# Kernel optimization log

Measured on AMD Instinct MI355X. Metric: run time of the kernel, lower is better.

Reference implementation:

```python
import jax, jax.numpy as jnp
import numpy as np

B, T, D, H, L, E, K = 4, 1024, 1024, 16, 2, 8, 2
HD = D // H                      # head_dim = 64
HALF = HD // 2                   # rope half dim = 32
CAP = int(np.ceil(2.0 * B * T / E))  # capacity factor 2 -> 1024
EPS = 1e-5


def build_sin_cos(seq_len, half_dim):
    pos = jnp.arange(seq_len, dtype=jnp.float32)[:, None]
    inv_freq = 1.0 / (10000.0 ** (jnp.arange(0, half_dim * 2, 2, dtype=jnp.float32) / (half_dim * 2)))
    ang = pos * inv_freq                      # (T, half_dim)
    return jnp.sin(ang), jnp.cos(ang)


def layernorm(x, g, b):
    mu = jnp.mean(x, -1, keepdims=True)
    var = jnp.mean(jnp.square(x - mu), -1, keepdims=True)
    return (x - mu) * jax.lax.rsqrt(var + EPS) * g + b


def attention(x, qkv_w, proj_w, sin, cos):
    # x: (B,T,D)
    qkv = (x @ qkv_w).reshape(B, T, H, 3 * HD)
    q, k, v = jnp.split(qkv, 3, axis=-1)      # each (B,T,H,HD)
    s = sin[None, :, None, :]                 # (1,T,1,HALF)
    c = cos[None, :, None, :]
    def rope(t):
        t1, t2 = t[..., :HALF], t[..., HALF:]
        return jnp.concatenate([t1 * c - t2 * s, t1 * s + t2 * c], axis=-1)
    q, k = rope(q), rope(k)
    scores = jnp.einsum('bqhd,bkhd->bhqk', q, k) / jnp.sqrt(jnp.float32(HD)).astype(x.dtype)
    causal = jnp.tril(jnp.ones((T, T), dtype=bool))
    scores = jnp.where(causal, scores, jnp.asarray(-1e9, scores.dtype))
    probs = jax.nn.softmax(scores, axis=-1)
    out = jnp.einsum('bhqk,bkhd->bqhd', probs, v).reshape(B, T, D)
    return out @ proj_w


def sparse_moe(x, gate_w, w1, b1, w2, b2):
    # eval mode: no router noise, aux_loss = 0
    flat = x.reshape(-1, D)                   # (N, D)
    N = flat.shape[0]
    gates = jax.nn.softmax((flat @ gate_w).astype(jnp.float32), axis=-1)  # (N, E)
    _, inds = jax.lax.top_k(gates, K)         # (N, K)
    mask = jnp.zeros((N, E), dtype=bool).at[jnp.arange(N)[:, None], inds].set(True)
    pos = jnp.cumsum(mask.astype(jnp.int32), axis=0) * mask - 1
    keep = (pos < CAP) & mask                 # (N, E) capacity-truncated assignment
    keepT = keep.T                            # (E, N)
    # stable argsort puts kept tokens first, preserving token order
    order = jnp.argsort(~keepT, axis=1)[:, :CAP]           # (E, CAP)
    valid = jnp.take_along_axis(keepT, order, axis=1)      # (E, CAP)
    safe = jnp.where(valid, order, 0)
    xg = flat[safe]                                        # (E, CAP, D)
    gv = jnp.take_along_axis(gates.T, safe, axis=1) * valid  # (E, CAP)
    h = jax.nn.gelu(jnp.einsum('ecd,edh->ech', xg, w1) + b1[:, None, :], approximate=False)
    out = jnp.einsum('ech,ehd->ecd', h, w2) + b2[:, None, :]
    contrib = out * gv[..., None].astype(flat.dtype)
    scatter_idx = jnp.where(valid, order, N)               # out-of-range -> dropped
    final = jnp.zeros_like(flat).at[scatter_idx.reshape(-1)].add(
        contrib.reshape(-1, D), mode='drop')
    return final.reshape(x.shape)


def setup_inputs() -> dict:
    key = jax.random.key(0)
    ks = jax.random.split(key, 8)
    s = 0.02
    return {
        'x': jax.random.normal(ks[0], (B, T, D), jnp.float32),
        'ln1_g': jnp.ones((L, D), jnp.float32),
        'ln1_b': jnp.zeros((L, D), jnp.float32),
        'qkv_w': jax.random.normal(ks[1], (L, D, 3 * D), jnp.float32) * s,
        'proj_w': jax.random.normal(ks[2], (L, D, D), jnp.float32) * s,
        'ln2_g': jnp.ones((L, D), jnp.float32),
        'ln2_b': jnp.zeros((L, D), jnp.float32),
        'gate_w': jax.random.normal(ks[3], (L, D, E), jnp.float32) * s,
        'w1': jax.random.normal(ks[4], (L, E, D, 4 * D), jnp.float32) * s,
        'b1': jnp.zeros((L, E, 4 * D), jnp.float32),
        'w2': jax.random.normal(ks[5], (L, E, 4 * D, D), jnp.float32) * s,
        'b2': jnp.zeros((L, E, D), jnp.float32),
    }


def reference(x, ln1_g, ln1_b, qkv_w, proj_w, ln2_g, ln2_b, gate_w, w1, b1, w2, b2):
    sin, cos = build_sin_cos(T, HALF)
    for l in range(L):
        x = x + attention(layernorm(x, ln1_g[l], ln1_b[l]), qkv_w[l], proj_w[l], sin, cos)
        x = x + sparse_moe(layernorm(x, ln2_g[l], ln2_b[l]), gate_w[l], w1[l], b1[l], w2[l], b2[l])
    return x
```

## Files before the change

### kernel.cpp

```cpp
#include <hip/hip_runtime.h>
#include <cstdint>

#define DD 1024
#define TT 1024
#define BB 4
#define HH 16
#define EE 8
#define NTOK 4096
#define CAPS 1024

using f16 = _Float16;
using f16x8 = __attribute__((ext_vector_type(8))) _Float16;
using f16x4 = __attribute__((ext_vector_type(4))) _Float16;
using f32x4 = __attribute__((ext_vector_type(4))) float;

#define MFMA16(a, b, c) __builtin_amdgcn_mfma_f32_16x16x32_f16(a, b, c, 0, 0, 0)

__device__ __forceinline__ void gload16(const void* g, void* l) {
  __builtin_amdgcn_global_load_lds((const __attribute__((address_space(1))) unsigned int*)g,
                                   (__attribute__((address_space(3))) unsigned int*)l, 16, 0, 0);
}

__device__ __forceinline__ void split2(float v, f16& h, f16& lo) {
  h = (f16)v;
  lo = (f16)((v - (float)h) * 2048.0f);
}

__device__ __forceinline__ void split_store(f16* ph, f16* pl, float v) {
  f16 h = (f16)v;
  *ph = h;
  *pl = (f16)((v - (float)h) * 2048.0f);
}

__global__ void splitT_k(const float* __restrict__ src, f16* __restrict__ dh, f16* __restrict__ dl,
                         int R, int C, long sSrc, long sDst) {
  __shared__ float tile[32][33];
  long z = blockIdx.z;
  src += z * sSrc; dh += z * sDst; dl += z * sDst;
  int c0 = blockIdx.x * 32, r0 = blockIdx.y * 32;
  int tx = threadIdx.x, ty = threadIdx.y;
  #pragma unroll
  for (int i = 0; i < 4; ++i) {
    int r = ty + i * 8;
    tile[r][tx] = src[(long)(r0 + r) * C + c0 + tx];
  }
  __syncthreads();
  #pragma unroll
  for (int i = 0; i < 4; ++i) {
    int cc = ty + i * 8;
    float v = tile[tx][cc];
    long idx = (long)(c0 + cc) * R + r0 + tx;
    f16 h, lo; split2(v, h, lo);
    dh[idx] = h; dl[idx] = lo;
  }
}

template<bool GATE>
__launch_bounds__(256)
__global__ void ln_k(const float* __restrict__ x, const float* __restrict__ g, const float* __restrict__ b,
                     f16* __restrict__ oh, f16* __restrict__ ol,
                     const float* __restrict__ gw, float* __restrict__ gates) {
  int row = blockIdx.x, tid = threadIdx.x;
  int lane = tid & 63, wid = tid >> 6;
  __shared__ float red[4];
  __shared__ float pg[4][8];
  __shared__ float logits[8];
  const float* xr = x + (long)row * DD;
  int col = tid * 4;
  float4 v = *(const float4*)(xr + col);
  float s = v.x + v.y + v.z + v.w;
  #pragma unroll
  for (int off = 32; off >= 1; off >>= 1) s += __shfl_down(s, off);
  if (lane == 0) red[wid] = s;
  __syncthreads();
  float mu = (red[0] + red[1] + red[2] + red[3]) * (1.0f / DD);
  float d0 = v.x - mu, d1 = v.y - mu, d2 = v.z - mu, d3 = v.w - mu;
  float sq = d0 * d0 + d1 * d1 + d2 * d2 + d3 * d3;
  __syncthreads();
  #pragma unroll
  for (int off = 32; off >= 1; off >>= 1) sq += __shfl_down(sq, off);
  if (lane == 0) red[wid] = sq;
  __syncthreads();
  float var = (red[0] + red[1] + red[2] + red[3]) * (1.0f / DD);
  float rstd = rsqrtf(var + 1e-5f);
  float xv[4];
  xv[0] = d0 * rstd * g[col] + b[col];
  xv[1] = d1 * rstd * g[col + 1] + b[col + 1];
  xv[2] = d2 * rstd * g[col + 2] + b[col + 2];
  xv[3] = d3 * rstd * g[col + 3] + b[col + 3];
  f16x4 hv, lv;
  #pragma unroll
  for (int j = 0; j < 4; ++j) { f16 h, lo; split2(xv[j], h, lo); hv[j] = h; lv[j] = lo; }
  *(f16x4*)(oh + (long)row * DD + col) = hv;
  *(f16x4*)(ol + (long)row * DD + col) = lv;
  if (GATE) {
    float part[8];
    #pragma unroll
    for (int e = 0; e < 8; ++e) part[e] = 0.0f;
    #pragma unroll
    for (int j = 0; j < 4; ++j) {
      const float* gwr = gw + (long)(col + j) * 8;
      #pragma unroll
      for (int e = 0; e < 8; ++e) part[e] += xv[j] * gwr[e];
    }
    #pragma unroll
    for (int off = 32; off >= 1; off >>= 1) {
      #pragma unroll
      for (int e = 0; e < 8; ++e) part[e] += __shfl_down(part[e], off);
    }
    if (lane == 0) {
      #pragma unroll
      for (int e = 0; e < 8; ++e) pg[wid][e] = part[e];
    }
    __syncthreads();
    if (tid < 8) logits[tid] = pg[0][tid] + pg[1][tid] + pg[2][tid] + pg[3][tid];
    __syncthreads();
    if (tid < 8) {
      float mx = logits[0];
      #pragma unroll
      for (int e2 = 1; e2 < 8; ++e2) mx = fmaxf(mx, logits[e2]);
      float den = 0.0f;
      #pragma unroll
      for (int e2 = 0; e2 < 8; ++e2) den += expf(logits[e2] - mx);
      gates[(long)row * 8 + tid] = expf(logits[tid] - mx) / den;
    }
  }
}

__global__ void sincos_k(float* st, float* ct) {
  int i = blockIdx.x * 256 + threadIdx.x;
  if (i >= TT * 32) return;
  int t = i >> 5, f = i & 31;
  float inv = powf(10000.0f, -(float)f * (1.0f / 32.0f));
  float ang = (float)t * inv;
  st[i] = sinf(ang);
  ct[i] = cosf(ang);
}

__launch_bounds__(256)
__global__ void rope_split_k(const float* __restrict__ qkv, const float* __restrict__ st, const float* __restrict__ ct,
                             f16* __restrict__ qh, f16* __restrict__ ql,
                             f16* __restrict__ kh, f16* __restrict__ kl,
                             f16* __restrict__ vth, f16* __restrict__ vtl) {
  int bx = blockIdx.x;
  int bh = bx >> 4, t0 = (bx & 15) * 64;
  int b = bh >> 4, hh = bh & 15;
  int tid = threadIdx.x;
  {
    int r = tid >> 2, quarter = tid & 3;
    int t = t0 + r;
    const float* rowp = qkv + ((long)(b * TT + t)) * 3072 + hh * 192;
    long obase = ((long)bh * TT + t) * 64;
    #pragma unroll
    for (int j = 0; j < 8; ++j) {
      int i = quarter * 8 + j;
      float sa = st[t * 32 + i], ca = ct[t * 32 + i];
      float a1 = rowp[i], a2 = rowp[i + 32];
      split_store(qh + obase + i, ql + obase + i, a1 * ca - a2 * sa);
      split_store(qh + obase + i + 32, ql + obase + i + 32, a1 * sa + a2 * ca);
      float c1 = rowp[64 + i], c2 = rowp[96 + i];
      split_store(kh + obase + i, kl + obase + i, c1 * ca - c2 * sa);
      split_store(kh + obase + i + 32, kl + obase + i + 32, c1 * sa + c2 * ca);
    }
  }
  __shared__ f16 vh_t[64][72];
  __shared__ f16 vl_t[64][72];
  {
    int d = tid & 63, tq = tid >> 6;
    #pragma unroll
    for (int p = 0; p < 16; ++p) {
      int tl = tq * 16 + p;
      float val = qkv[((long)(b * TT + t0 + tl)) * 3072 + hh * 192 + 128 + d];
      f16 h, lo; split2(val, h, lo);
      vh_t[tl][d] = h; vl_t[tl][d] = lo;
    }
  }
  __syncthreads();
  {
    int d = tid >> 2, c = tid & 3;
    long vbase = ((long)bh * 64 + d) * TT + t0 + c * 16;
    f16x8 ph0, ph1, pl0, pl1;
    #pragma unroll
    for (int j = 0; j < 8; ++j) {
      ph0[j] = vh_t[c * 16 + j][d];
      pl0[j] = vl_t[c * 16 + j][d];
      ph1[j] = vh_t[c * 16 + 8 + j][d];
      pl1[j] = vl_t[c * 16 + 8 + j][d];
    }
    *(f16x8*)(vth + vbase) = ph0;
    *(f16x8*)(vth + vbase + 8) = ph1;
    *(f16x8*)(vtl + vbase) = pl0;
    *(f16x8*)(vtl + vbase + 8) = pl1;
  }
}

__launch_bounds__(256)
__global__ void attn_k(const f16* __restrict__ qh, const f16* __restrict__ ql,
                       const f16* __restrict__ kh, const f16* __restrict__ kl,
                       const f16* __restrict__ vth, const f16* __restrict__ vtl,
                       f16* __restrict__ oh_out, f16* __restrict__ ol_out) {
  int bx = blockIdx.x;
  int bh = bx >> 4, qt = bx & 15;
  int tid = threadIdx.x;
  int wid = tid >> 6, lane = tid & 63;
  int lr = lane & 15, lg = lane >> 4;
  int qbase = qt * 64 + wid * 16;
  long bhT = (long)bh * TT;

  long qoff = (bhT + qbase + lr) * 64 + lg * 8;
  f16x8 q_h0 = *(const f16x8*)(qh + qoff);
  f16x8 q_h1 = *(const f16x8*)(qh + qoff + 32);
  f16x8 q_l0 = *(const f16x8*)(ql + qoff);
  f16x8 q_l1 = *(const f16x8*)(ql + qoff + 32);

  f32x4 o_hi[4], o_md[4];
  #pragma unroll
  for (int d = 0; d < 4; ++d) {
    o_hi[d] = {0.f, 0.f, 0.f, 0.f};
    o_md[d] = {0.f, 0.f, 0.f, 0.f};
  }
  float m[4], lsum[4];
  #pragma unroll
  for (int j = 0; j < 4; ++j) { m[j] = -1e30f; lsum[j] = 0.0f; }

  __shared__ f16 Ph[4][16][32];
  __shared__ f16 Pl[4][16][32];

  int ntiles = (qbase + 47) >> 5;
  for (int kb = 0; kb < ntiles; ++kb) {
    int kv0 = kb * 32;
    float sv[2][4];
    #pragma unroll
    for (int ni = 0; ni < 2; ++ni) {
      long koff = (bhT + kv0 + ni * 16 + lr) * 64 + lg * 8;
      f16x8 k_h0 = *(const f16x8*)(kh + koff);
      f16x8 k_h1 = *(const f16x8*)(kh + koff + 32);
      f16x8 k_l0 = *(const f16x8*)(kl + koff);
      f16x8 k_l1 = *(const f16x8*)(kl + koff + 32);
      f32x4 a = {0.f, 0.f, 0.f, 0.f};
      a = MFMA16(q_h0, k_h0, a);
      a = MFMA16(q_h1, k_h1, a);
      a = a * 2048.0f;
      a = MFMA16(q_h0, k_l0, a);
      a = MFMA16(q_h1, k_l1, a);
      a = MFMA16(q_l0, k_h0, a);
      a = MFMA16(q_l1, k_h1, a);
      #pragma unroll
      for (int j = 0; j < 4; ++j) sv[ni][j] = a[j];
    }
    const float sscale = 0.125f / 2048.0f;
    bool needmask = (kv0 + 32 > qbase);
    float rm[4];
    #pragma unroll
    for (int j = 0; j < 4; ++j) {
      int qrow = qbase + lg * 4 + j;
      float s0 = sv[0][j] * sscale;
      float s1 = sv[1][j] * sscale;
      if (needmask) {
        if (kv0 + lr > qrow) s0 = -1e9f;
        if (kv0 + 16 + lr > qrow) s1 = -1e9f;
      }
      sv[0][j] = s0; sv[1][j] = s1;
      rm[j] = fmaxf(s0, s1);
    }
    #pragma unroll
    for (int off = 1; off < 16; off <<= 1) {
      #pragma unroll
      for (int j = 0; j < 4; ++j) rm[j] = fmaxf(rm[j], __shfl_xor(rm[j], off));
    }
    float alpha[4], rs[4];
    #pragma unroll
    for (int j = 0; j < 4; ++j) {
      float mn = fmaxf(m[j], rm[j]);
      alpha[j] = expf(m[j] - mn);
      m[j] = mn;
      float p0 = expf(sv[0][j] - mn);
      float p1 = expf(sv[1][j] - mn);
      sv[0][j] = p0; sv[1][j] = p1;
      rs[j] = p0 + p1;
    }
    #pragma unroll
    for (int off = 1; off < 16; off <<= 1) {
      #pragma unroll
      for (int j = 0; j < 4; ++j) rs[j] += __shfl_xor(rs[j], off);
    }
    #pragma unroll
    for (int j = 0; j < 4; ++j) lsum[j] = lsum[j] * alpha[j] + rs[j];
    #pragma unroll
    for (int d = 0; d < 4; ++d) {
      #pragma unroll
      for (int j = 0; j < 4; ++j) { o_hi[d][j] *= alpha[j]; o_md[d][j] *= alpha[j]; }
    }
    #pragma unroll
    for (int ni = 0; ni < 2; ++ni) {
      #pragma unroll
      for (int j = 0; j < 4; ++j) {
        float pv = sv[ni][j];
        f16 hv = (f16)pv;
        Ph[wid][lg * 4 + j][ni * 16 + lr] = hv;
        Pl[wid][lg * 4 + j][ni * 16 + lr] = (f16)((pv - (float)hv) * 2048.0f);
      }
    }
    f16x8 pa_h = *(const f16x8*)(&Ph[wid][lr][lg * 8]);
    f16x8 pa_l = *(const f16x8*)(&Pl[wid][lr][lg * 8]);
    #pragma unroll
    for (int d = 0; d < 4; ++d) {
      long voff = ((long)bh * 64 + d * 16 + lr) * TT + kv0 + lg * 8;
      f16x8 v_h = *(const f16x8*)(vth + voff);
      f16x8 v_l = *(const f16x8*)(vtl + voff);
      o_hi[d] = MFMA16(pa_h, v_h, o_hi[d]);
      o_md[d] = MFMA16(pa_h, v_l, o_md[d]);
      o_md[d] = MFMA16(pa_l, v_h, o_md[d]);
    }
  }
  int b = bh >> 4, hh = bh & 15;
  #pragma unroll
  for (int j = 0; j < 4; ++j) {
    float invl = 1.0f / lsum[j];
    int qrow = qbase + lg * 4 + j;
    long obase = ((long)(b * TT + qrow)) * DD + hh * 64 + lr;
    #pragma unroll
    for (int d = 0; d < 4; ++d) {
      float val = (o_hi[d][j] + o_md[d][j] * (1.0f / 2048.0f)) * invl;
      f16 hv = (f16)val;
      oh_out[obase + d * 16] = hv;
      ol_out[obase + d * 16] = (f16)((val - (float)hv) * 2048.0f);
    }
  }
}

template<int EPI, bool SPLIT>
__launch_bounds__(256, 2)
__global__ void gemmF(const f16* __restrict__ Ah, const f16* __restrict__ Al, long sA,
                      const f16* __restrict__ Bh, const f16* __restrict__ Bl, long sB,
                      int M, int N, int K,
                      float* __restrict__ outF, long sOutF,
                      const float* __restrict__ resid,
                      const float* __restrict__ bias, long sBias,
                      f16* __restrict__ outH, f16* __restrict__ outL, long sOutH) {
  __shared__ __align__(16) f16 pool[(SPLIT ? 4 : 2) * 128 * 64];
  f16* AsH = pool;
  f16* BsH = pool + 8192;
  f16* AsL = SPLIT ? pool + 16384 : pool;
  f16* BsL = SPLIT ? pool + 24576 : pool;

  int z = blockIdx.z;
  int bn = blockIdx.x, bm = blockIdx.y;
  int tid = threadIdx.x;
  int wid = tid >> 6, lane = tid & 63;
  int wm = (wid >> 1) * 64, wn = (wid & 1) * 64;
  int lr = lane & 15, lg = lane >> 4;

  f32x4 aH[4][4], aL[4][4];
  #pragma unroll
  for (int i = 0; i < 4; ++i)
    #pragma unroll
    for (int j = 0; j < 4; ++j) {
      aH[i][j] = {0.f, 0.f, 0.f, 0.f};
      if (SPLIT) aL[i][j] = {0.f, 0.f, 0.f, 0.f};
    }

  int srow = tid >> 3;
  int gcol = (((tid & 7) ^ (srow & 7)) << 3);
  const f16* apH = Ah + (long)z * sA + ((long)(bm * 128 + srow)) * K + gcol;
  const f16* bpH = Bh + (long)z * sB + ((long)(bn * 128 + srow)) * K + gcol;
  const f16* apL = nullptr; const f16* bpL = nullptr;
  if (SPLIT) {
    apL = Al + (long)z * sA + ((long)(bm * 128 + srow)) * K + gcol;
    bpL = Bl + (long)z * sB + ((long)(bn * 128 + srow)) * K + gcol;
  }
  int tid8 = tid * 8;
  int rsw = lr & 7;

  for (int kt = 0; kt < K; kt += 64) {
    #pragma unroll
    for (int r4 = 0; r4 < 4; ++r4) {
      long go = (long)kt + (long)(r4 * 32) * K;
      int lo = tid8 + r4 * 2048;
      gload16(apH + go, AsH + lo);
      gload16(bpH + go, BsH + lo);
      if (SPLIT) {
        gload16(apL + go, AsL + lo);
        gload16(bpL + go, BsL + lo);
      }
    }
    __syncthreads();
    #pragma unroll
    for (int kk2 = 0; kk2 < 2; ++kk2) {
      int sws = (((kk2 << 2) | lg) ^ rsw) << 3;
      f16x8 afH[4], afL[4];
      #pragma unroll
      for (int i = 0; i < 4; ++i) {
        int ro = (wm + i * 16 + lr) * 64 + sws;
        afH[i] = *(const f16x8*)(AsH + ro);
        if (SPLIT) afL[i] = *(const f16x8*)(AsL + ro);
      }
      #pragma unroll
      for (int j = 0; j < 4; ++j) {
        int ro = (wn + j * 16 + lr) * 64 + sws;
        f16x8 bH = *(const f16x8*)(BsH + ro);
        #pragma unroll
        for (int i = 0; i < 4; ++i) aH[i][j] = MFMA16(afH[i], bH, aH[i][j]);
        if (SPLIT) {
          f16x8 bL = *(const f16x8*)(BsL + ro);
          #pragma unroll
          for (int i = 0; i < 4; ++i) {
            aL[i][j] = MFMA16(afH[i], bL, aL[i][j]);
            aL[i][j] = MFMA16(afL[i], bH, aL[i][j]);
          }
        }
      }
    }
    __syncthreads();
  }

  #pragma unroll
  for (int i = 0; i < 4; ++i) {
    #pragma unroll
    for (int j = 0; j < 4; ++j) {
      #pragma unroll
      for (int r = 0; r < 4; ++r) {
        int row = bm * 128 + wm + i * 16 + lg * 4 + r;
        int col = bn * 128 + wn + j * 16 + lr;
        float v = aH[i][j][r];
        if (SPLIT) v += aL[i][j][r] * (1.0f / 2048.0f);
        if (EPI == 0) {
          outF[(long)row * N + col] = v;
        } else if (EPI == 1) {
          long idx = (long)row * N + col;
          outF[idx] = v + resid[idx];
        } else if (EPI == 2) {
          float t = v + bias[(long)z * sBias + col];
          float ge = 0.5f * t * (1.0f + erff(t * 0.70710678118f));
          long idx = (long)z * sOutH + (long)row * N + col;
          f16 hv = (f16)ge;
          outH[idx] = hv;
          if (SPLIT) outL[idx] = (f16)((ge - (float)hv) * 2048.0f);
        } else {
          long idx = (long)z * sOutF + (long)row * N + col;
          outF[idx] = v + bias[(long)z * sBias + col];
        }
      }
    }
  }
}

__launch_bounds__(512)
__global__ void route_k(const float* __restrict__ gates, int* __restrict__ etok, int* __restrict__ slotof) {
  __shared__ unsigned char lmask[NTOK];
  __shared__ unsigned char ltop[NTOK];
  int tid = threadIdx.x;
  for (int t = tid; t < NTOK; t += 512) {
    const float* gr = gates + (long)t * 8;
    float gv[8];
    #pragma unroll
    for (int e = 0; e < 8; ++e) gv[e] = gr[e];
    int e1 = 0; float bv = gv[0];
    #pragma unroll
    for (int e = 1; e < 8; ++e) if (gv[e] > bv) { bv = gv[e]; e1 = e; }
    int e2 = -1; float bv2 = -1e30f;
    #pragma unroll
    for (int e = 0; e < 8; ++e) if (e != e1 && gv[e] > bv2) { bv2 = gv[e]; e2 = e; }
    lmask[t] = (unsigned char)((1u << e1) | (1u << e2));
    ltop[t] = (unsigned char)(e1 | (e2 << 4));
    slotof[t * 2] = -1;
    slotof[t * 2 + 1] = -1;
  }
  __syncthreads();
  int e = tid >> 6, lane = tid & 63;
  int cnt = 0;
  for (int c = 0; c < NTOK / 64; ++c) {
    int t = c * 64 + lane;
    int bit = (lmask[t] >> e) & 1;
    unsigned long long bal = __ballot(bit);
    int pre = __popcll(bal & ((1ull << lane) - 1ull));
    int slot = cnt + pre;
    if (bit && slot < CAPS) {
      etok[e * CAPS + slot] = t;
      int tp = ltop[t];
      int k = ((tp & 15) == e) ? 0 : 1;
      slotof[t * 2 + k] = (e << 16) | slot;
    }
    cnt += __popcll(bal);
  }
  int kept = cnt < CAPS ? cnt : CAPS;
  for (int s = kept + lane; s < CAPS; s += 64) etok[e * CAPS + s] = 0;
}

__global__ void gather_k(const int* __restrict__ etok, const f16* __restrict__ xh, const f16* __restrict__ xl,
                         f16* __restrict__ gh, f16* __restrict__ gl) {
  int es = blockIdx.x, tid = threadIdx.x;
  int tok = etok[es];
  const uint4* s1 = (const uint4*)(xh + (long)tok * DD);
  const uint4* s2 = (const uint4*)(xl + (long)tok * DD);
  ((uint4*)(gh + (long)es * DD))[tid] = s1[tid];
  ((uint4*)(gl + (long)es * DD))[tid] = s2[tid];
}

__global__ void scatter_k(const int* __restrict__ slotof, const float* __restrict__ gates,
                          const float* __restrict__ moe, float* __restrict__ x) {
  int t = blockIdx.x, tid = threadIdx.x;
  int s0 = slotof[t * 2], s1 = slotof[t * 2 + 1];
  float4* xr = (float4*)(x + (long)t * DD);
  float4 v = xr[tid];
  if (s0 >= 0) {
    int e = s0 >> 16, sl = s0 & 0xffff;
    float gv = gates[(long)t * 8 + e];
    float4 mo = ((const float4*)(moe + ((long)e * CAPS + sl) * DD))[tid];
    v.x += gv * mo.x; v.y += gv * mo.y; v.z += gv * mo.z; v.w += gv * mo.w;
  }
  if (s1 >= 0) {
    int e = s1 >> 16, sl = s1 & 0xffff;
    float gv = gates[(long)t * 8 + e];
    float4 mo = ((const float4*)(moe + ((long)e * CAPS + sl) * DD))[tid];
    v.x += gv * mo.x; v.y += gv * mo.y; v.z += gv * mo.z; v.w += gv * mo.w;
  }
  xr[tid] = v;
}

extern "C" void kernel_launch(void* const* d_in, const int* in_sizes, int n_in,
                              void* d_out, int out_size, void* d_ws, size_t ws_size,
                              hipStream_t stream) {
  const float* x_in   = (const float*)d_in[0];
  const float* ln1_g  = (const float*)d_in[1];
  const float* ln1_b  = (const float*)d_in[2];
  const float* qkv_w  = (const float*)d_in[3];
  const float* proj_w = (const float*)d_in[4];
  const float* ln2_g  = (const float*)d_in[5];
  const float* ln2_b  = (const float*)d_in[6];
  const float* gate_w = (const float*)d_in[7];
  const float* w1     = (const float*)d_in[8];
  const float* b1     = (const float*)d_in[9];
  const float* w2     = (const float*)d_in[10];
  const float* b2     = (const float*)d_in[11];
  float* x = (float*)d_out;

  char* p = (char*)d_ws;
  auto alloc = [&](size_t bytes) { char* r = p; p += (bytes + 255) & ~(size_t)255; return (void*)r; };

  f16* Wreg   = (f16*)alloc(134217728);
  float* qkvb = (float*)alloc(4096ull * 3072 * 4);
  f16* qhB  = (f16*)alloc(4194304ull * 2);
  f16* qlB  = (f16*)alloc(4194304ull * 2);
  f16* khB  = (f16*)alloc(4194304ull * 2);
  f16* klB  = (f16*)alloc(4194304ull * 2);
  f16* vthB = (f16*)alloc(4194304ull * 2);
  f16* vtlB = (f16*)alloc(4194304ull * 2);
  f16* xnh  = (f16*)alloc(4194304ull * 2);
  f16* xnl  = (f16*)alloc(4194304ull * 2);
  f16* atth = (f16*)alloc(4194304ull * 2);
  f16* attl = (f16*)alloc(4194304ull * 2);
  f16* xgh  = (f16*)alloc(8388608ull * 2);
  f16* xgl  = (f16*)alloc(8388608ull * 2);
  f16* hhB  = (f16*)alloc(33554432ull * 2);
  f16* hlB  = (f16*)alloc(33554432ull * 2);
  float* moe = (float*)alloc(8388608ull * 4);
  float* stab = (float*)alloc(32768ull * 4);
  float* ctab = (float*)alloc(32768ull * 4);
  float* gates = (float*)alloc(32768ull * 4);
  int* etok  = (int*)alloc(8192ull * 4);
  int* slotof = (int*)alloc(8192ull * 4);

  f16* qkvTh = Wreg;
  f16* qkvTl = Wreg + 3145728;
  f16* projTh = Wreg + 2 * 3145728;
  f16* projTl = Wreg + 2 * 3145728 + 1048576;
  f16* w1Th = Wreg;
  f16* w1Tl = Wreg + 33554432;
  f16* w2Th = Wreg;
  f16* w2Tl = Wreg + 33554432;

  hipMemcpyAsync(x, x_in, (size_t)NTOK * DD * 4, hipMemcpyDeviceToDevice, stream);
  sincos_k<<<(TT * 32 + 255) / 256, 256, 0, stream>>>(stab, ctab);

  for (int l = 0; l < 2; ++l) {
    splitT_k<<<dim3(3072 / 32, 1024 / 32, 1), dim3(32, 8), 0, stream>>>(
        qkv_w + (long)l * DD * 3072, qkvTh, qkvTl, 1024, 3072, 0, 0);
    splitT_k<<<dim3(1024 / 32, 1024 / 32, 1), dim3(32, 8), 0, stream>>>(
        proj_w + (long)l * DD * DD, projTh, projTl, 1024, 1024, 0, 0);
    ln_k<false><<<NTOK, 256, 0, stream>>>(x, ln1_g + l * DD, ln1_b + l * DD, xnh, xnl, nullptr, nullptr);
    gemmF<0, true><<<dim3(3072 / 128, 4096 / 128, 1), 256, 0, stream>>>(
        xnh, xnl, 0, qkvTh, qkvTl, 0, 4096, 3072, 1024,
        qkvb, 0, nullptr, nullptr, 0, nullptr, nullptr, 0);
    rope_split_k<<<BB * HH * (TT / 64), 256, 0, stream>>>(qkvb, stab, ctab, qhB, qlB, khB, klB, vthB, vtlB);
    attn_k<<<BB * HH * (TT / 64), 256, 0, stream>>>(qhB, qlB, khB, klB, vthB, vtlB, atth, attl);
    gemmF<1, true><<<dim3(1024 / 128, 4096 / 128, 1), 256, 0, stream>>>(
        atth, attl, 0, projTh, projTl, 0, 4096, 1024, 1024,
        x, 0, x, nullptr, 0, nullptr, nullptr, 0);

    ln_k<true><<<NTOK, 256, 0, stream>>>(x, ln2_g + l * DD, ln2_b + l * DD, xnh, xnl,
                                         gate_w + (long)l * DD * EE, gates);
    route_k<<<1, 512, 0, stream>>>(gates, etok, slotof);
    gather_k<<<EE * CAPS, 128, 0, stream>>>(etok, xnh, xnl, xgh, xgl);
    splitT_k<<<dim3(4096 / 32, 1024 / 32, EE), dim3(32, 8), 0, stream>>>(
        w1 + (long)l * EE * DD * 4096, w1Th, w1Tl, 1024, 4096, (long)DD * 4096, (long)4096 * DD);
    if (l == 0) {
      gemmF<2, true><<<dim3(4096 / 128, 1024 / 128, EE), 256, 0, stream>>>(
          xgh, xgl, (long)CAPS * DD, w1Th, w1Tl, (long)4096 * DD, 1024, 4096, 1024,
          nullptr, 0, nullptr, b1 + (long)l * EE * 4096, 4096, hhB, hlB, (long)CAPS * 4096);
    } else {
      gemmF<2, false><<<dim3(4096 / 128, 1024 / 128, EE), 256, 0, stream>>>(
          xgh, xgl, (long)CAPS * DD, w1Th, w1Tl, (long)4096 * DD, 1024, 4096, 1024,
          nullptr, 0, nullptr, b1 + (long)l * EE * 4096, 4096, hhB, hlB, (long)CAPS * 4096);
    }
    splitT_k<<<dim3(1024 / 32, 4096 / 32, EE), dim3(32, 8), 0, stream>>>(
        w2 + (long)l * EE * 4096 * DD, w2Th, w2Tl, 4096, 1024, (long)4096 * DD, (long)DD * 4096);
    if (l == 0) {
      gemmF<3, true><<<dim3(1024 / 128, 1024 / 128, EE), 256, 0, stream>>>(
          hhB, hlB, (long)CAPS * 4096, w2Th, w2Tl, (long)DD * 4096, 1024, 1024, 4096,
          moe, (long)CAPS * DD, nullptr, b2 + (long)l * EE * DD, DD, nullptr, nullptr, 0);
    } else {
      gemmF<3, false><<<dim3(1024 / 128, 1024 / 128, EE), 256, 0, stream>>>(
          hhB, hlB, (long)CAPS * 4096, w2Th, w2Tl, (long)DD * 4096, 1024, 1024, 4096,
          moe, (long)CAPS * DD, nullptr, b2 + (long)l * EE * DD, DD, nullptr, nullptr, 0);
    }
    scatter_k<<<NTOK, 256, 0, stream>>>(slotof, gates, moe, x);
  }
  (void)in_sizes; (void)n_in; (void)out_size; (void)ws_size;
}
```

Measured before the change: 1.758 ms.

## Restructure attention to stage K/V tiles in LDS with larger query tiles

Rewrites the flash-attention kernel so each block handles 128 query rows (32 per wave) and loads 64-key K/V tiles cooperatively into swizzled LDS through async global-to-LDS loads. Every staged K/V tile is then reused by all four waves instead of each wave reading K/V from global memory directly. Blocks are ordered with a permuted query-tile mapping to balance causal work, and the exponentials switch to the fast __expf. In exchange the kernel pays for two block-wide barriers per tile and higher register and LDS use, and the grid shrinks to 512 blocks.

```diff
diff --git a/kernel.cpp b/kernel.cpp
--- a/kernel.cpp
+++ b/kernel.cpp
@@ -194,139 +194,208 @@
   }
 }
 
-__launch_bounds__(256)
+__launch_bounds__(256, 2)
 __global__ void attn_k(const f16* __restrict__ qh, const f16* __restrict__ ql,
                        const f16* __restrict__ kh, const f16* __restrict__ kl,
                        const f16* __restrict__ vth, const f16* __restrict__ vtl,
                        f16* __restrict__ oh_out, f16* __restrict__ ol_out) {
+  __shared__ __align__(16) f16 KsH[4096], KsL[4096], VsH[4096], VsL[4096];
+  __shared__ __align__(16) f16 Pw[4][2][2048];
   int bx = blockIdx.x;
-  int bh = bx >> 4, qt = bx & 15;
+  int bh = bx & 63;
+  int qt = (int)((0x31204657u >> ((bx >> 6) << 2)) & 7u);
   int tid = threadIdx.x;
   int wid = tid >> 6, lane = tid & 63;
   int lr = lane & 15, lg = lane >> 4;
-  int qbase = qt * 64 + wid * 16;
   long bhT = (long)bh * TT;
-
-  long qoff = (bhT + qbase + lr) * 64 + lg * 8;
-  f16x8 q_h0 = *(const f16x8*)(qh + qoff);
-  f16x8 q_h1 = *(const f16x8*)(qh + qoff + 32);
-  f16x8 q_l0 = *(const f16x8*)(ql + qoff);
-  f16x8 q_l1 = *(const f16x8*)(ql + qoff + 32);
-
-  f32x4 o_hi[4], o_md[4];
-  #pragma unroll
-  for (int d = 0; d < 4; ++d) {
-    o_hi[d] = {0.f, 0.f, 0.f, 0.f};
-    o_md[d] = {0.f, 0.f, 0.f, 0.f};
-  }
-  float m[4], lsum[4];
-  #pragma unroll
-  for (int j = 0; j < 4; ++j) { m[j] = -1e30f; lsum[j] = 0.0f; }
-
-  __shared__ f16 Ph[4][16][32];
-  __shared__ f16 Pl[4][16][32];
-
-  int ntiles = (qbase + 47) >> 5;
+  int qrow0 = qt * 128 + wid * 32;
+  int qend = qrow0 + 32;
+
+  f16x8 qfh[2][2], qfl[2][2];
+  #pragma unroll
+  for (int qi = 0; qi < 2; ++qi) {
+    long qoff = (bhT + qrow0 + qi * 16 + lr) * 64 + lg * 8;
+    qfh[qi][0] = *(const f16x8*)(qh + qoff);
+    qfh[qi][1] = *(const f16x8*)(qh + qoff + 32);
+    qfl[qi][0] = *(const f16x8*)(ql + qoff);
+    qfl[qi][1] = *(const f16x8*)(ql + qoff + 32);
+  }
+
+  f32x4 o_hi[2][4], o_md[2][4];
+  #pragma unroll
+  for (int qi = 0; qi < 2; ++qi)
+    #pragma unroll
+    for (int dj = 0; dj < 4; ++dj) {
+      o_hi[qi][dj] = {0.f, 0.f, 0.f, 0.f};
+      o_md[qi][dj] = {0.f, 0.f, 0.f, 0.f};
+    }
+  float m[2][4], lsum[2][4];
+  #pragma unroll
+  for (int qi = 0; qi < 2; ++qi)
+    #pragma unroll
+    for (int r = 0; r < 4; ++r) { m[qi][r] = -1e30f; lsum[qi][r] = 0.0f; }
+
+  int srow = tid >> 3, slot = tid & 7;
+  int gc = ((slot ^ (srow & 7)) << 3);
+  const f16* kHp = kh + (bhT + srow) * 64 + gc;
+  const f16* kLp = kl + (bhT + srow) * 64 + gc;
+  const f16* vHp = vth + ((long)bh * 64 + srow) * TT + gc;
+  const f16* vLp = vtl + ((long)bh * 64 + srow) * TT + gc;
+  int t8 = tid * 8;
+  int rsw = lr & 7;
+  int c0 = ((lg ^ rsw) << 3), c1 = (((4 | lg) ^ rsw) << 3);
+  f16* Ph = Pw[wid][0];
+  f16* Pl = Pw[wid][1];
+
+  int ntiles = 2 * (qt + 1);
   for (int kb = 0; kb < ntiles; ++kb) {
-    int kv0 = kb * 32;
-    float sv[2][4];
-    #pragma unroll
-    for (int ni = 0; ni < 2; ++ni) {
-      long koff = (bhT + kv0 + ni * 16 + lr) * 64 + lg * 8;
-      f16x8 k_h0 = *(const f16x8*)(kh + koff);
-      f16x8 k_h1 = *(const f16x8*)(kh + koff + 32);
-      f16x8 k_l0 = *(const f16x8*)(kl + koff);
-      f16x8 k_l1 = *(const f16x8*)(kl + koff + 32);
-      f32x4 a = {0.f, 0.f, 0.f, 0.f};
-      a = MFMA16(q_h0, k_h0, a);
-      a = MFMA16(q_h1, k_h1, a);
-      a = a * 2048.0f;
-      a = MFMA16(q_h0, k_l0, a);
-      a = MFMA16(q_h1, k_l1, a);
-      a = MFMA16(q_l0, k_h0, a);
-      a = MFMA16(q_l1, k_h1, a);
-      #pragma unroll
-      for (int j = 0; j < 4; ++j) sv[ni][j] = a[j];
-    }
-    const float sscale = 0.125f / 2048.0f;
-    bool needmask = (kv0 + 32 > qbase);
-    float rm[4];
-    #pragma unroll
-    for (int j = 0; j < 4; ++j) {
-      int qrow = qbase + lg * 4 + j;
-      float s0 = sv[0][j] * sscale;
-      float s1 = sv[1][j] * sscale;
-      if (needmask) {
-        if (kv0 + lr > qrow) s0 = -1e9f;
-        if (kv0 + 16 + lr > qrow) s1 = -1e9f;
-      }
-      sv[0][j] = s0; sv[1][j] = s1;
-      rm[j] = fmaxf(s0, s1);
-    }
-    #pragma unroll
-    for (int off = 1; off < 16; off <<= 1) {
-      #pragma unroll
-      for (int j = 0; j < 4; ++j) rm[j] = fmaxf(rm[j], __shfl_xor(rm[j], off));
-    }
-    float alpha[4], rs[4];
-    #pragma unroll
-    for (int j = 0; j < 4; ++j) {
-      float mn = fmaxf(m[j], rm[j]);
-      alpha[j] = expf(m[j] - mn);
-      m[j] = mn;
-      float p0 = expf(sv[0][j] - mn);
-      float p1 = expf(sv[1][j] - mn);
-      sv[0][j] = p0; sv[1][j] = p1;
-      rs[j] = p0 + p1;
-    }
-    #pragma unroll
-    for (int off = 1; off < 16; off <<= 1) {
-      #pragma unroll
-      for (int j = 0; j < 4; ++j) rs[j] += __shfl_xor(rs[j], off);
-    }
-    #pragma unroll
-    for (int j = 0; j < 4; ++j) lsum[j] = lsum[j] * alpha[j] + rs[j];
-    #pragma unroll
-    for (int d = 0; d < 4; ++d) {
-      #pragma unroll
-      for (int j = 0; j < 4; ++j) { o_hi[d][j] *= alpha[j]; o_md[d][j] *= alpha[j]; }
-    }
-    #pragma unroll
-    for (int ni = 0; ni < 2; ++ni) {
-      #pragma unroll
-      for (int j = 0; j < 4; ++j) {
-        float pv = sv[ni][j];
-        f16 hv = (f16)pv;
-        Ph[wid][lg * 4 + j][ni * 16 + lr] = hv;
-        Pl[wid][lg * 4 + j][ni * 16 + lr] = (f16)((pv - (float)hv) * 2048.0f);
-      }
-    }
-    f16x8 pa_h = *(const f16x8*)(&Ph[wid][lr][lg * 8]);
-    f16x8 pa_l = *(const f16x8*)(&Pl[wid][lr][lg * 8]);
-    #pragma unroll
-    for (int d = 0; d < 4; ++d) {
-      long voff = ((long)bh * 64 + d * 16 + lr) * TT + kv0 + lg * 8;
-      f16x8 v_h = *(const f16x8*)(vth + voff);
-      f16x8 v_l = *(const f16x8*)(vtl + voff);
-      o_hi[d] = MFMA16(pa_h, v_h, o_hi[d]);
-      o_md[d] = MFMA16(pa_h, v_l, o_md[d]);
-      o_md[d] = MFMA16(pa_l, v_h, o_md[d]);
-    }
-  }
+    int kv0 = kb * 64;
+    gload16(kHp + (long)kv0 * 64, KsH + t8);
+    gload16(kHp + (long)(kv0 + 32) * 64, KsH + 2048 + t8);
+    gload16(kLp + (long)kv0 * 64, KsL + t8);
+    gload16(kLp + (long)(kv0 + 32) * 64, KsL + 2048 + t8);
+    gload16(vHp + kv0, VsH + t8);
+    gload16(vHp + (long)32 * TT + kv0, VsH + 2048 + t8);
+    gload16(vLp + kv0, VsL + t8);
+    gload16(vLp + (long)32 * TT + kv0, VsL + 2048 + t8);
+    __syncthreads();
+
+    if (kv0 < qend) {
+      f32x4 s[2][4];
+      #pragma unroll
+      for (int kj = 0; kj < 4; ++kj) {
+        int rb = (kj * 16 + lr) * 64;
+        f16x8 kfh0 = *(const f16x8*)(KsH + rb + c0);
+        f16x8 kfh1 = *(const f16x8*)(KsH + rb + c1);
+        f16x8 kfl0 = *(const f16x8*)(KsL + rb + c0);
+        f16x8 kfl1 = *(const f16x8*)(KsL + rb + c1);
+        #pragma unroll
+        for (int qi = 0; qi < 2; ++qi) {
+          f32x4 a = {0.f, 0.f, 0.f, 0.f};
+          a = MFMA16(qfh[qi][0], kfh0, a);
+          a = MFMA16(qfh[qi][1], kfh1, a);
+          a = a * 2048.0f;
+          a = MFMA16(qfh[qi][0], kfl0, a);
+          a = MFMA16(qfh[qi][1], kfl1, a);
+          a = MFMA16(qfl[qi][0], kfh0, a);
+          a = MFMA16(qfl[qi][1], kfh1, a);
+          s[qi][kj] = a;
+        }
+      }
+      const float ss = 0.125f / 2048.0f;
+      bool needmask = (kv0 + 64 > qrow0);
+      float rm[2][4];
+      #pragma unroll
+      for (int qi = 0; qi < 2; ++qi)
+        #pragma unroll
+        for (int r = 0; r < 4; ++r) {
+          int qrow = qrow0 + qi * 16 + lg * 4 + r;
+          float mx = -1e30f;
+          #pragma unroll
+          for (int kj = 0; kj < 4; ++kj) {
+            float v = s[qi][kj][r] * ss;
+            if (needmask && (kv0 + kj * 16 + lr > qrow)) v = -1e9f;
+            s[qi][kj][r] = v;
+            mx = fmaxf(mx, v);
+          }
+          rm[qi][r] = mx;
+        }
+      #pragma unroll
+      for (int off = 1; off < 16; off <<= 1)
+        #pragma unroll
+        for (int qi = 0; qi < 2; ++qi)
+          #pragma unroll
+          for (int r = 0; r < 4; ++r) rm[qi][r] = fmaxf(rm[qi][r], __shfl_xor(rm[qi][r], off));
+      float alpha[2][4], rs[2][4];
+      #pragma unroll
+      for (int qi = 0; qi < 2; ++qi)
+        #pragma unroll
+        for (int r = 0; r < 4; ++r) {
+          float mn = fmaxf(m[qi][r], rm[qi][r]);
+          alpha[qi][r] = __expf(m[qi][r] - mn);
+          m[qi][r] = mn;
+          rs[qi][r] = 0.0f;
+        }
+      #pragma unroll
+      for (int qi = 0; qi < 2; ++qi)
+        #pragma unroll
+        for (int kj = 0; kj < 4; ++kj)
+          #pragma unroll
+          for (int r = 0; r < 4; ++r) {
+            float p = __expf(s[qi][kj][r] - m[qi][r]);
+            rs[qi][r] += p;
+            int prow = qi * 16 + lg * 4 + r;
+            int pcol = kj * 16 + lr;
+            int idx = prow * 64 + (((pcol >> 3) ^ (prow & 7)) << 3) + (pcol & 7);
+            f16 hv = (f16)p;
+            Ph[idx] = hv;
+            Pl[idx] = (f16)((p - (float)hv) * 2048.0f);
+          }
+      #pragma unroll
+      for (int off = 1; off < 16; off <<= 1)
+        #pragma unroll
+        for (int qi = 0; qi < 2; ++qi)
+          #pragma unroll
+          for (int r = 0; r < 4; ++r) rs[qi][r] += __shfl_xor(rs[qi][r], off);
+      #pragma unroll
+      for (int qi = 0; qi < 2; ++qi)
+        #pragma unroll
+        for (int r = 0; r < 4; ++r) lsum[qi][r] = lsum[qi][r] * alpha[qi][r] + rs[qi][r];
+      #pragma unroll
+      for (int qi = 0; qi < 2; ++qi)
+        #pragma unroll
+        for (int dj = 0; dj < 4; ++dj)
+          #pragma unroll
+          for (int r = 0; r < 4; ++r) {
+            o_hi[qi][dj][r] *= alpha[qi][r];
+            o_md[qi][dj][r] *= alpha[qi][r];
+          }
+      f16x8 pah[2][2], pal[2][2];
+      #pragma unroll
+      for (int qi = 0; qi < 2; ++qi) {
+        int pr = (qi * 16 + lr) * 64;
+        pah[qi][0] = *(const f16x8*)(Ph + pr + c0);
+        pah[qi][1] = *(const f16x8*)(Ph + pr + c1);
+        pal[qi][0] = *(const f16x8*)(Pl + pr + c0);
+        pal[qi][1] = *(const f16x8*)(Pl + pr + c1);
+      }
+      #pragma unroll
+      for (int dj = 0; dj < 4; ++dj) {
+        int vb = (dj * 16 + lr) * 64;
+        f16x8 vh0 = *(const f16x8*)(VsH + vb + c0);
+        f16x8 vh1 = *(const f16x8*)(VsH + vb + c1);
+        f16x8 vl0 = *(const f16x8*)(VsL + vb + c0);
+        f16x8 vl1 = *(const f16x8*)(VsL + vb + c1);
+        #pragma unroll
+        for (int qi = 0; qi < 2; ++qi) {
+          o_hi[qi][dj] = MFMA16(pah[qi][0], vh0, o_hi[qi][dj]);
+          o_hi[qi][dj] = MFMA16(pah[qi][1], vh1, o_hi[qi][dj]);
+          o_md[qi][dj] = MFMA16(pah[qi][0], vl0, o_md[qi][dj]);
+          o_md[qi][dj] = MFMA16(pah[qi][1], vl1, o_md[qi][dj]);
+          o_md[qi][dj] = MFMA16(pal[qi][0], vh0, o_md[qi][dj]);
+          o_md[qi][dj] = MFMA16(pal[qi][1], vh1, o_md[qi][dj]);
+        }
+      }
+    }
+    __syncthreads();
+  }
+
   int b = bh >> 4, hh = bh & 15;
   #pragma unroll
-  for (int j = 0; j < 4; ++j) {
-    float invl = 1.0f / lsum[j];
-    int qrow = qbase + lg * 4 + j;
-    long obase = ((long)(b * TT + qrow)) * DD + hh * 64 + lr;
-    #pragma unroll
-    for (int d = 0; d < 4; ++d) {
-      float val = (o_hi[d][j] + o_md[d][j] * (1.0f / 2048.0f)) * invl;
-      f16 hv = (f16)val;
-      oh_out[obase + d * 16] = hv;
-      ol_out[obase + d * 16] = (f16)((val - (float)hv) * 2048.0f);
-    }
-  }
+  for (int qi = 0; qi < 2; ++qi)
+    #pragma unroll
+    for (int r = 0; r < 4; ++r) {
+      float invl = 1.0f / lsum[qi][r];
+      int qrow = qrow0 + qi * 16 + lg * 4 + r;
+      long obase = ((long)(b * TT + qrow)) * DD + hh * 64 + lr;
+      #pragma unroll
+      for (int dj = 0; dj < 4; ++dj) {
+        float val = (o_hi[qi][dj][r] + o_md[qi][dj][r] * (1.0f / 2048.0f)) * invl;
+        f16 hv = (f16)val;
+        oh_out[obase + dj * 16] = hv;
+        ol_out[obase + dj * 16] = (f16)((val - (float)hv) * 2048.0f);
+      }
+    }
 }
 
 template<int EPI, bool SPLIT>
@@ -583,7 +652,7 @@
         xnh, xnl, 0, qkvTh, qkvTl, 0, 4096, 3072, 1024,
         qkvb, 0, nullptr, nullptr, 0, nullptr, nullptr, 0);
     rope_split_k<<<BB * HH * (TT / 64), 256, 0, stream>>>(qkvb, stab, ctab, qhB, qlB, khB, klB, vthB, vtlB);
-    attn_k<<<BB * HH * (TT / 64), 256, 0, stream>>>(qhB, qlB, khB, klB, vthB, vtlB, atth, attl);
+    attn_k<<<512, 256, 0, stream>>>(qhB, qlB, khB, klB, vthB, vtlB, atth, attl);
     gemmF<1, true><<<dim3(1024 / 128, 4096 / 128, 1), 256, 0, stream>>>(
         atth, attl, 0, projTh, projTl, 0, 4096, 1024, 1024,
         x, 0, x, nullptr, 0, nullptr, nullptr, 0);
```

Result: faster. 1.458 ms (-17.1%).
